# Performance work log

Hardware: AMD Instinct MI355X
Metric: run time of the kernel (lower is better)

Reference implementation:

```python
import jax, jax.numpy as jnp
import numpy as np

L, T, F, DIM = 16, 16384, 2, 3
N_MIN, N_MAX = 16.0, 512.0
N_PTS = 262144
# torch code builds np.int32 primes [1, 2654435761, 805459861]; 2654435761 wraps to -1640531535.
# Since T is a power of two, int32 wraparound multiply/xor followed by nonnegative mod T gives
# bit-identical indices to the int64 torch computation.
PIS = jnp.array([1, -1640531535, 805459861], dtype=jnp.int32)
# corner ordering from get_indices: corner k = a*4+b*2+c with a->dim0, b->dim1, c->dim2
OFFS = jnp.array([[(k >> 2) & 1, (k >> 1) & 1, k & 1] for k in range(8)], dtype=jnp.float32)  # (8,3)


def setup_inputs() -> dict:
    key = jax.random.key(0)
    k1, k2 = jax.random.split(key)
    x = jax.random.uniform(k1, (N_PTS, DIM), dtype=jnp.float32)
    # nn.init.uniform_(weight, a=-1e-4, b=1e-4) for each of L tables of shape (T, F)
    embeddings = jax.random.uniform(k2, (L, T, F), minval=-1e-4, maxval=1e-4, dtype=jnp.float32)
    return {"x": x, "embeddings": embeddings}


def reference(x, embeddings):
    # per-level growth factor b = exp((log Nmax - log Nmin)/L); N_l = Nmin * b**l
    b = jnp.exp((jnp.log(N_MAX) - jnp.log(N_MIN)) / L)
    N_l = N_MIN * b ** jnp.arange(L, dtype=jnp.float32)                      # (L,)
    un_x = x[None, :, :] * N_l[:, None, None]                                # (L,N,3)  (mu=0, sigma=1)
    lo = jnp.floor(un_x)
    hi = jnp.ceil(un_x)
    d = hi - lo                                                              # (L,N,3)
    nz = d != 0
    diff = jnp.where(nz, (un_x - lo) / jnp.where(nz, d, 1.0), 0.0)           # (L,N,3)

    mask = OFFS.astype(bool)[None, None]                                     # (1,1,8,3)
    corners = jnp.where(mask, hi[:, :, None, :], lo[:, :, None, :])          # (L,N,8,3)
    ci = corners.astype(jnp.int32)
    prod = ci * PIS                                                          # (L,N,8,3) wrapping int32 mul
    idx = jnp.mod(prod[..., 0] ^ prod[..., 1] ^ prod[..., 2], T)             # (L,N,8)

    # per-level table gather: (L,T,F)[ (L,N,8) ] -> (L,N,8,F)
    feats = jax.vmap(lambda emb, i: emb[i])(embeddings, idx)

    # trilinear weights: prod over dims of (diff if corner bit else 1-diff)
    w = jnp.prod(jnp.where(mask, diff[:, :, None, :], 1.0 - diff[:, :, None, :]), axis=-1)  # (L,N,8)
    c = jnp.einsum('lnc,lncf->lnf', w, feats)                                # (L,N,F)
    return jnp.transpose(c, (1, 0, 2)).reshape(x.shape[0], L * F)            # (N, L*F)
```

## Files before the change

kernel.cpp:

```cpp
#include <hip/hip_runtime.h>
#include <stdint.h>

constexpr int L_LEVELS = 16;
constexpr int T_SIZE   = 16384;
constexpr int N_PTS    = 262144;

typedef _Float16 h2 __attribute__((ext_vector_type(2)));
typedef _Float16 h4 __attribute__((ext_vector_type(4)));
typedef _Float16 h8 __attribute__((ext_vector_type(8)));

constexpr uint32_t P1_4 = 2654435761u * 4u;
constexpr uint32_t P2_4 = 805459861u * 4u;
constexpr uint32_t M4   = (T_SIZE - 1) * 4u;

__device__ __forceinline__ h2 lerp2(h2 a, h2 b, h2 t) {
    return a + t * (b - a);
}


__global__ __launch_bounds__(256) void cvt_tables(
    const float* __restrict__ emb, h2* __restrict__ tbl)
{
    const int i = blockIdx.x * 256 + threadIdx.x;
    const float4* __restrict__ s = reinterpret_cast<const float4*>(emb);
    float4 a = s[2 * i];
    float4 b = s[2 * i + 1];
    h8 w = { (_Float16)a.x, (_Float16)a.y, (_Float16)a.z, (_Float16)a.w,
             (_Float16)b.x, (_Float16)b.y, (_Float16)b.z, (_Float16)b.w };
    reinterpret_cast<h8*>(tbl)[i] = w;
}

__global__ __launch_bounds__(512, 4) void hash_encode_level(
    const float* __restrict__ x,
    const h2*    __restrict__ tbl,
    h2*          __restrict__ res)
{
    __shared__ h2 tab[T_SIZE];

    const int t     = threadIdx.x;
    const int l     = blockIdx.x & (L_LEVELS - 1);
    const int chunk = blockIdx.x >> 4;
    const int n0    = chunk * 4096 + t * 8;

    {
        const h8* __restrict__ s =
            reinterpret_cast<const h8*>(tbl + (size_t)l * T_SIZE);
        h8* __restrict__ d = reinterpret_cast<h8*>(tab);
#pragma unroll
        for (int r = 0; r < 8; ++r) {
            const int j = r * 512 + t;
            d[j] = s[j];
        }
    }

    union { float4 q[6]; float f[24]; } xs;
    {
        const float4* __restrict__ xv =
            reinterpret_cast<const float4*>(x + (size_t)n0 * 3);
#pragma unroll
        for (int i = 0; i < 6; ++i) xs.q[i] = xv[i];
    }
    __syncthreads();

    const float Nl = 16.0f * exp2f((float)l * 0.3125f);
    const char* __restrict__ tb = reinterpret_cast<const char*>(tab);

    union { h2 r[8]; float4 q[2]; } out8;

#pragma unroll
    for (int p = 0; p < 8; ++p) {
        const float u0 = xs.f[3 * p + 0] * Nl;
        const float u1 = xs.f[3 * p + 1] * Nl;
        const float u2 = xs.f[3 * p + 2] * Nl;

        const float fl0 = floorf(u0), fl1 = floorf(u1), fl2 = floorf(u2);
        const float df0 = u0 - fl0, df1 = u1 - fl1, df2 = u2 - fl2;

        const uint32_t q0 = ((uint32_t)(int32_t)fl0) << 2;
        const uint32_t q1 = ((uint32_t)(int32_t)fl1) * P1_4;
        const uint32_t q2 = ((uint32_t)(int32_t)fl2) * P2_4;
        const uint32_t d0 = (q0 ^ (q0 + 4u))   & M4;
        const uint32_t d1 = (q1 ^ (q1 + P1_4)) & M4;
        const uint32_t d2 = (q2 ^ (q2 + P2_4)) & M4;

        uint32_t off = (q0 ^ q1 ^ q2) & M4;

        constexpr int gray[8] = {0, 1, 3, 2, 6, 7, 5, 4};
        h2 f[8];
#pragma unroll
        for (int j = 0; j < 8; ++j) {
            f[gray[j]] = *reinterpret_cast<const h2*>(tb + off);
            if (j < 7) {
                const int tog = gray[j] ^ gray[j + 1];
                off ^= (tog == 4) ? d0 : (tog == 2) ? d1 : d2;
            }
        }

        const _Float16 h0 = (_Float16)df0, h1 = (_Float16)df1,
                       hv2 = (_Float16)df2;
        const h2 t0 = {h0, h0}, t1 = {h1, h1}, t2 = {hv2, hv2};
        h2 e0 = lerp2(f[0], f[1], t2);
        h2 e1 = lerp2(f[2], f[3], t2);
        h2 e2 = lerp2(f[4], f[5], t2);
        h2 e3 = lerp2(f[6], f[7], t2);
        h2 g0 = lerp2(e0, e1, t1);
        h2 g1 = lerp2(e2, e3, t1);
        out8.r[p] = lerp2(g0, g1, t0);
    }

    {
        float4* __restrict__ o4 = reinterpret_cast<float4*>(
            res + (size_t)l * N_PTS + n0);
        o4[0] = out8.q[0];
        o4[1] = out8.q[1];
    }
}

__global__ __launch_bounds__(256) void transpose_expand(
    const h2* __restrict__ res,
    float4*   __restrict__ out)
{
    __shared__ h2 tile[L_LEVELS][514];
    const int t    = threadIdx.x;
    const int base = blockIdx.x * 512;

#pragma unroll
    for (int l = 0; l < L_LEVELS; ++l) {
        h4 v = reinterpret_cast<const h4*>(res + (size_t)l * N_PTS + base)[t];
        *reinterpret_cast<h4*>(&tile[l][2 * t]) = v;
    }
    __syncthreads();

    float4* __restrict__ o = out + (size_t)base * 8;
#pragma unroll
    for (int i = 0; i < L_LEVELS; ++i) {
        const int f    = i * 256 + t;
        const int p    = f >> 3;
        const int part = f & 7;
        h2 a = tile[2 * part][p];
        h2 b = tile[2 * part + 1][p];
        o[f] = make_float4((float)a.x, (float)a.y,
                           (float)b.x, (float)b.y);
    }
}

__global__ __launch_bounds__(1024, 4) void hash_encode_fused(
    const float* __restrict__ x,
    const float* __restrict__ emb,
    float4*      __restrict__ out)
{
    __shared__ union {
        h2 tab[2][T_SIZE];
        h2 tr[1024][20];
    } sm;

    const int t = threadIdx.x;
    const int n = blockIdx.x * 1024 + t;
    const int rot = (blockIdx.x << 4) & 4095;

    const float x0 = x[3 * n + 0];
    const float x1 = x[3 * n + 1];
    const float x2 = x[3 * n + 2];

    {
        const float4* __restrict__ s = reinterpret_cast<const float4*>(emb);
        h8* __restrict__ d = reinterpret_cast<h8*>(sm.tab[0]);
#pragma unroll
        for (int r = 0; r < 4; ++r) {
            const int j = (r * 1024 + t + rot) & 4095;
            float4 a = s[2 * j];
            float4 b = s[2 * j + 1];
            h8 w = { (_Float16)a.x, (_Float16)a.y, (_Float16)a.z, (_Float16)a.w,
                     (_Float16)b.x, (_Float16)b.y, (_Float16)b.z, (_Float16)b.w };
            d[j] = w;
        }
    }
    __syncthreads();

    union { h2 r[L_LEVELS]; h8 q[4]; } resu;

#pragma unroll
    for (int l = 0; l < L_LEVELS; ++l) {
        float4 sa0, sb0, sa1, sb1, sa2, sb2, sa3, sb3;
        int j0 = 0, j1 = 0, j2 = 0, j3 = 0;
        if (l < L_LEVELS - 1) {
            const float4* __restrict__ s = reinterpret_cast<const float4*>(
                emb + (size_t)(l + 1) * T_SIZE * 2);
            j0 = (0 * 1024 + t + rot) & 4095;
            j1 = (1 * 1024 + t + rot) & 4095;
            j2 = (2 * 1024 + t + rot) & 4095;
            j3 = (3 * 1024 + t + rot) & 4095;
            sa0 = s[2 * j0]; sb0 = s[2 * j0 + 1];
            sa1 = s[2 * j1]; sb1 = s[2 * j1 + 1];
            sa2 = s[2 * j2]; sb2 = s[2 * j2 + 1];
            sa3 = s[2 * j3]; sb3 = s[2 * j3 + 1];
        }

        const float Nl = 16.0f * exp2f((float)l * 0.3125f);
        const char* __restrict__ tb =
            reinterpret_cast<const char*>(sm.tab[l & 1]);

        const float u0 = x0 * Nl, u1 = x1 * Nl, u2 = x2 * Nl;
        const float fl0 = floorf(u0), fl1 = floorf(u1), fl2 = floorf(u2);
        const float df0 = u0 - fl0, df1 = u1 - fl1, df2 = u2 - fl2;

        const uint32_t q0 = ((uint32_t)(int32_t)fl0) << 2;
        const uint32_t q1 = ((uint32_t)(int32_t)fl1) * P1_4;
        const uint32_t q2 = ((uint32_t)(int32_t)fl2) * P2_4;
        const uint32_t d0 = (q0 ^ (q0 + 4u))   & M4;
        const uint32_t d1 = (q1 ^ (q1 + P1_4)) & M4;
        const uint32_t d2 = (q2 ^ (q2 + P2_4)) & M4;

        uint32_t off = (q0 ^ q1 ^ q2) & M4;

        constexpr int gray[8] = {0, 1, 3, 2, 6, 7, 5, 4};
        h2 f[8];
#pragma unroll
        for (int j = 0; j < 8; ++j) {
            f[gray[j]] = *reinterpret_cast<const h2*>(tb + off);
            if (j < 7) {
                const int tog = gray[j] ^ gray[j + 1];
                off ^= (tog == 4) ? d0 : (tog == 2) ? d1 : d2;
            }
        }

        const _Float16 h0 = (_Float16)df0, h1 = (_Float16)df1, hv2 = (_Float16)df2;
        const h2 t0 = {h0, h0}, t1 = {h1, h1}, t2 = {hv2, hv2};
        h2 e0 = lerp2(f[0], f[1], t2);
        h2 e1 = lerp2(f[2], f[3], t2);
        h2 e2 = lerp2(f[4], f[5], t2);
        h2 e3 = lerp2(f[6], f[7], t2);
        h2 g0 = lerp2(e0, e1, t1);
        h2 g1 = lerp2(e2, e3, t1);
        resu.r[l] = lerp2(g0, g1, t0);

        if (l < L_LEVELS - 1) {
            h8* __restrict__ d = reinterpret_cast<h8*>(sm.tab[(l + 1) & 1]);
            h8 w0 = { (_Float16)sa0.x, (_Float16)sa0.y, (_Float16)sa0.z, (_Float16)sa0.w,
                      (_Float16)sb0.x, (_Float16)sb0.y, (_Float16)sb0.z, (_Float16)sb0.w };
            h8 w1 = { (_Float16)sa1.x, (_Float16)sa1.y, (_Float16)sa1.z, (_Float16)sa1.w,
                      (_Float16)sb1.x, (_Float16)sb1.y, (_Float16)sb1.z, (_Float16)sb1.w };
            h8 w2 = { (_Float16)sa2.x, (_Float16)sa2.y, (_Float16)sa2.z, (_Float16)sa2.w,
                      (_Float16)sb2.x, (_Float16)sb2.y, (_Float16)sb2.z, (_Float16)sb2.w };
            h8 w3 = { (_Float16)sa3.x, (_Float16)sa3.y, (_Float16)sa3.z, (_Float16)sa3.w,
                      (_Float16)sb3.x, (_Float16)sb3.y, (_Float16)sb3.z, (_Float16)sb3.w };
            d[j0] = w0;
            d[j1] = w1;
            d[j2] = w2;
            d[j3] = w3;
            __syncthreads();
        }
    }

    __syncthreads();
#pragma unroll
    for (int g = 0; g < 4; ++g)
        *reinterpret_cast<h8*>(&sm.tr[t][4 * g]) = resu.q[g];
    __syncthreads();

    float4* __restrict__ o = out + (size_t)blockIdx.x * 8192;
#pragma unroll
    for (int i = 0; i < 8; ++i) {
        const int p  = i * 128 + (t >> 3);
        const int l0 = 2 * (t & 7);
        h4 v = *reinterpret_cast<const h4*>(&sm.tr[p][l0]);
        o[i * 1024 + t] = make_float4((float)v.x, (float)v.y,
                                      (float)v.z, (float)v.w);
    }
}

extern "C" void kernel_launch(void* const* d_in, const int* in_sizes, int n_in,
                              void* d_out, int out_size, void* d_ws, size_t ws_size,
                              hipStream_t stream) {
    const float* x   = (const float*)d_in[0];
    const float* emb = (const float*)d_in[1];

    const size_t RES_OFF = (size_t)2 << 20;
    const size_t need    = RES_OFF + (size_t)L_LEVELS * N_PTS * sizeof(h2);

    if (ws_size >= need) {
        h2* tbl = (h2*)d_ws;
        h2* res = (h2*)((char*)d_ws + RES_OFF);
        cvt_tables<<<256, 256, 0, stream>>>(emb, tbl);
        hash_encode_level<<<1024, 512, 0, stream>>>(x, tbl, res);
        transpose_expand<<<512, 256, 0, stream>>>(res, (float4*)d_out);
    } else {
        hash_encode_fused<<<256, 1024, 0, stream>>>(x, emb, (float4*)d_out);
    }
}
```

Baseline: 87.38 us.

## Fuse fp16 table conversion into LDS fill and pair point lookups

```diff
diff --git a/kernel.cpp b/kernel.cpp
--- a/kernel.cpp
+++ b/kernel.cpp
@@ -18,38 +18,30 @@
 }
 
 
-__global__ __launch_bounds__(256) void cvt_tables(
-    const float* __restrict__ emb, h2* __restrict__ tbl)
-{
-    const int i = blockIdx.x * 256 + threadIdx.x;
-    const float4* __restrict__ s = reinterpret_cast<const float4*>(emb);
-    float4 a = s[2 * i];
-    float4 b = s[2 * i + 1];
-    h8 w = { (_Float16)a.x, (_Float16)a.y, (_Float16)a.z, (_Float16)a.w,
-             (_Float16)b.x, (_Float16)b.y, (_Float16)b.z, (_Float16)b.w };
-    reinterpret_cast<h8*>(tbl)[i] = w;
-}
-
-__global__ __launch_bounds__(512, 4) void hash_encode_level(
+__global__ __launch_bounds__(512, 4) void hash_encode_lds(
     const float* __restrict__ x,
-    const h2*    __restrict__ tbl,
+    const float* __restrict__ emb,
     h2*          __restrict__ res)
 {
     __shared__ h2 tab[T_SIZE];
 
-    const int t     = threadIdx.x;
     const int l     = blockIdx.x & (L_LEVELS - 1);
     const int chunk = blockIdx.x >> 4;
+    const int t     = threadIdx.x;
     const int n0    = chunk * 4096 + t * 8;
 
     {
-        const h8* __restrict__ s =
-            reinterpret_cast<const h8*>(tbl + (size_t)l * T_SIZE);
-        h8* __restrict__ d = reinterpret_cast<h8*>(tab);
-#pragma unroll
-        for (int r = 0; r < 8; ++r) {
-            const int j = r * 512 + t;
-            d[j] = s[j];
+        const float4* __restrict__ src =
+            reinterpret_cast<const float4*>(emb + (size_t)l * T_SIZE * 2);
+        h8* __restrict__ d8 = reinterpret_cast<h8*>(tab);
+#pragma unroll
+        for (int it = 0; it < 8; ++it) {
+            const int i = it * 512 + t;
+            float4 a = src[2 * i];
+            float4 b = src[2 * i + 1];
+            h8 w = { (_Float16)a.x, (_Float16)a.y, (_Float16)a.z, (_Float16)a.w,
+                     (_Float16)b.x, (_Float16)b.y, (_Float16)b.z, (_Float16)b.w };
+            d8[i] = w;
         }
     }
 
@@ -68,44 +60,59 @@
     union { h2 r[8]; float4 q[2]; } out8;
 
 #pragma unroll
-    for (int p = 0; p < 8; ++p) {
-        const float u0 = xs.f[3 * p + 0] * Nl;
-        const float u1 = xs.f[3 * p + 1] * Nl;
-        const float u2 = xs.f[3 * p + 2] * Nl;
-
-        const float fl0 = floorf(u0), fl1 = floorf(u1), fl2 = floorf(u2);
-        const float df0 = u0 - fl0, df1 = u1 - fl1, df2 = u2 - fl2;
-
-        const uint32_t q0 = ((uint32_t)(int32_t)fl0) << 2;
-        const uint32_t q1 = ((uint32_t)(int32_t)fl1) * P1_4;
-        const uint32_t q2 = ((uint32_t)(int32_t)fl2) * P2_4;
-        const uint32_t d0 = (q0 ^ (q0 + 4u))   & M4;
-        const uint32_t d1 = (q1 ^ (q1 + P1_4)) & M4;
-        const uint32_t d2 = (q2 ^ (q2 + P2_4)) & M4;
-
-        uint32_t off = (q0 ^ q1 ^ q2) & M4;
-
-        constexpr int gray[8] = {0, 1, 3, 2, 6, 7, 5, 4};
-        h2 f[8];
-#pragma unroll
-        for (int j = 0; j < 8; ++j) {
-            f[gray[j]] = *reinterpret_cast<const h2*>(tb + off);
-            if (j < 7) {
-                const int tog = gray[j] ^ gray[j + 1];
-                off ^= (tog == 4) ? d0 : (tog == 2) ? d1 : d2;
+    for (int pp = 0; pp < 8; pp += 2) {
+        uint32_t off[2], dd0[2], dd1[2], dd2[2];
+        h2 tt0[2], tt1[2], tt2[2];
+#pragma unroll
+        for (int k = 0; k < 2; ++k) {
+            const int p = pp + k;
+            const float u0 = xs.f[3 * p + 0] * Nl;
+            const float u1 = xs.f[3 * p + 1] * Nl;
+            const float u2 = xs.f[3 * p + 2] * Nl;
+
+            const float fl0 = floorf(u0), fl1 = floorf(u1), fl2 = floorf(u2);
+            const float df0 = u0 - fl0, df1 = u1 - fl1, df2 = u2 - fl2;
+
+            const uint32_t q0 = ((uint32_t)(int32_t)fl0) << 2;
+            const uint32_t q1 = ((uint32_t)(int32_t)fl1) * P1_4;
+            const uint32_t q2 = ((uint32_t)(int32_t)fl2) * P2_4;
+            dd0[k] = (q0 ^ (q0 + 4u))   & M4;
+            dd1[k] = (q1 ^ (q1 + P1_4)) & M4;
+            dd2[k] = (q2 ^ (q2 + P2_4)) & M4;
+            off[k] = (q0 ^ q1 ^ q2) & M4;
+
+            const _Float16 h0 = (_Float16)df0, h1 = (_Float16)df1,
+                           hv2 = (_Float16)df2;
+            tt0[k] = h2{h0, h0};
+            tt1[k] = h2{h1, h1};
+            tt2[k] = h2{hv2, hv2};
+        }
+
+        h2 f[2][8];
+#pragma unroll
+        for (int k = 0; k < 2; ++k) {
+            constexpr int gray[8] = {0, 1, 3, 2, 6, 7, 5, 4};
+            uint32_t o = off[k];
+#pragma unroll
+            for (int j = 0; j < 8; ++j) {
+                f[k][gray[j]] = *reinterpret_cast<const h2*>(tb + o);
+                if (j < 7) {
+                    const int tog = gray[j] ^ gray[j + 1];
+                    o ^= (tog == 4) ? dd0[k] : (tog == 2) ? dd1[k] : dd2[k];
+                }
             }
         }
 
-        const _Float16 h0 = (_Float16)df0, h1 = (_Float16)df1,
-                       hv2 = (_Float16)df2;
-        const h2 t0 = {h0, h0}, t1 = {h1, h1}, t2 = {hv2, hv2};
-        h2 e0 = lerp2(f[0], f[1], t2);
-        h2 e1 = lerp2(f[2], f[3], t2);
-        h2 e2 = lerp2(f[4], f[5], t2);
-        h2 e3 = lerp2(f[6], f[7], t2);
-        h2 g0 = lerp2(e0, e1, t1);
-        h2 g1 = lerp2(e2, e3, t1);
-        out8.r[p] = lerp2(g0, g1, t0);
+#pragma unroll
+        for (int k = 0; k < 2; ++k) {
+            h2 e0 = lerp2(f[k][0], f[k][1], tt2[k]);
+            h2 e1 = lerp2(f[k][2], f[k][3], tt2[k]);
+            h2 e2 = lerp2(f[k][4], f[k][5], tt2[k]);
+            h2 e3 = lerp2(f[k][6], f[k][7], tt2[k]);
+            h2 g0 = lerp2(e0, e1, tt1[k]);
+            h2 g1 = lerp2(e2, e3, tt1[k]);
+            out8.r[pp + k] = lerp2(g0, g1, tt0[k]);
+        }
     }
 
     {
@@ -275,14 +282,11 @@
     const float* x   = (const float*)d_in[0];
     const float* emb = (const float*)d_in[1];
 
-    const size_t RES_OFF = (size_t)2 << 20;
-    const size_t need    = RES_OFF + (size_t)L_LEVELS * N_PTS * sizeof(h2);
+    const size_t need = (size_t)L_LEVELS * N_PTS * sizeof(h2);
 
     if (ws_size >= need) {
-        h2* tbl = (h2*)d_ws;
-        h2* res = (h2*)((char*)d_ws + RES_OFF);
-        cvt_tables<<<256, 256, 0, stream>>>(emb, tbl);
-        hash_encode_level<<<1024, 512, 0, stream>>>(x, tbl, res);
+        h2* res = (h2*)d_ws;
+        hash_encode_lds<<<1024, 512, 0, stream>>>(x, emb, res);
         transpose_expand<<<512, 256, 0, stream>>>(res, (float4*)d_out);
     } else {
         hash_encode_fused<<<256, 1024, 0, stream>>>(x, emb, (float4*)d_out);
```

New measurement: 87.29 us. No clear change (-0.1%).

## Fuse level encode and transpose into one kernel with async LDS table staging

Applied to the files above, without the earlier changes.

```diff
diff --git a/kernel.cpp b/kernel.cpp
--- a/kernel.cpp
+++ b/kernel.cpp
@@ -30,49 +30,52 @@
     reinterpret_cast<h8*>(tbl)[i] = w;
 }
 
-__global__ __launch_bounds__(512, 4) void hash_encode_level(
+__global__ __launch_bounds__(1024, 4) void hash_encode_dma(
     const float* __restrict__ x,
     const h2*    __restrict__ tbl,
-    h2*          __restrict__ res)
+    float4*      __restrict__ out)
 {
-    __shared__ h2 tab[T_SIZE];
-
-    const int t     = threadIdx.x;
-    const int l     = blockIdx.x & (L_LEVELS - 1);
-    const int chunk = blockIdx.x >> 4;
-    const int n0    = chunk * 4096 + t * 8;
-
-    {
-        const h8* __restrict__ s =
-            reinterpret_cast<const h8*>(tbl + (size_t)l * T_SIZE);
-        h8* __restrict__ d = reinterpret_cast<h8*>(tab);
-#pragma unroll
-        for (int r = 0; r < 8; ++r) {
-            const int j = r * 512 + t;
-            d[j] = s[j];
-        }
-    }
-
-    union { float4 q[6]; float f[24]; } xs;
-    {
-        const float4* __restrict__ xv =
-            reinterpret_cast<const float4*>(x + (size_t)n0 * 3);
-#pragma unroll
-        for (int i = 0; i < 6; ++i) xs.q[i] = xv[i];
-    }
-    __syncthreads();
-
-    const float Nl = 16.0f * exp2f((float)l * 0.3125f);
-    const char* __restrict__ tb = reinterpret_cast<const char*>(tab);
-
-    union { h2 r[8]; float4 q[2]; } out8;
-
-#pragma unroll
-    for (int p = 0; p < 8; ++p) {
-        const float u0 = xs.f[3 * p + 0] * Nl;
-        const float u1 = xs.f[3 * p + 1] * Nl;
-        const float u2 = xs.f[3 * p + 2] * Nl;
-
+    __shared__ union {
+        h2 tab[2][T_SIZE];
+        h2 tr[1024][18];
+    } sm;
+
+    const int t    = threadIdx.x;
+    const int lane = t & 63;
+    const int wid  = t >> 6;
+    const int n    = blockIdx.x * 1024 + t;
+
+    const float x0 = x[3 * n + 0];
+    const float x1 = x[3 * n + 1];
+    const float x2 = x[3 * n + 2];
+
+    const char* __restrict__ gt = reinterpret_cast<const char*>(tbl);
+
+    auto stage = [&](int lvl, int b) {
+        const char* g = gt + ((size_t)lvl << 16) + (wid << 12) + (lane << 4);
+        char* d = reinterpret_cast<char*>(sm.tab[b]) + (wid << 12);
+#pragma unroll
+        for (int it = 0; it < 4; ++it)
+            __builtin_amdgcn_global_load_lds(
+                (const __attribute__((address_space(1))) void*)(g + (it << 10)),
+                (__attribute__((address_space(3))) void*)(d + (it << 10)),
+                16, 0, 0);
+    };
+
+    stage(0, 0);
+    __syncthreads();
+
+    union { h2 r[L_LEVELS]; h4 q4[8]; } res;
+
+#pragma unroll
+    for (int l = 0; l < L_LEVELS; ++l) {
+        if (l < L_LEVELS - 1) stage(l + 1, (l + 1) & 1);
+
+        const float Nl = 16.0f * exp2f((float)l * 0.3125f);
+        const char* __restrict__ tb =
+            reinterpret_cast<const char*>(sm.tab[l & 1]);
+
+        const float u0 = x0 * Nl, u1 = x1 * Nl, u2 = x2 * Nl;
         const float fl0 = floorf(u0), fl1 = floorf(u1), fl2 = floorf(u2);
         const float df0 = u0 - fl0, df1 = u1 - fl1, df2 = u2 - fl2;
 
@@ -105,42 +108,25 @@
         h2 e3 = lerp2(f[6], f[7], t2);
         h2 g0 = lerp2(e0, e1, t1);
         h2 g1 = lerp2(e2, e3, t1);
-        out8.r[p] = lerp2(g0, g1, t0);
-    }
-
-    {
-        float4* __restrict__ o4 = reinterpret_cast<float4*>(
-            res + (size_t)l * N_PTS + n0);
-        o4[0] = out8.q[0];
-        o4[1] = out8.q[1];
-    }
-}
-
-__global__ __launch_bounds__(256) void transpose_expand(
-    const h2* __restrict__ res,
-    float4*   __restrict__ out)
-{
-    __shared__ h2 tile[L_LEVELS][514];
-    const int t    = threadIdx.x;
-    const int base = blockIdx.x * 512;
-
-#pragma unroll
-    for (int l = 0; l < L_LEVELS; ++l) {
-        h4 v = reinterpret_cast<const h4*>(res + (size_t)l * N_PTS + base)[t];
-        *reinterpret_cast<h4*>(&tile[l][2 * t]) = v;
-    }
-    __syncthreads();
-
-    float4* __restrict__ o = out + (size_t)base * 8;
-#pragma unroll
-    for (int i = 0; i < L_LEVELS; ++i) {
-        const int f    = i * 256 + t;
+        res.r[l] = lerp2(g0, g1, t0);
+
+        __syncthreads();
+    }
+
+#pragma unroll
+    for (int g = 0; g < 8; ++g)
+        *reinterpret_cast<h4*>(&sm.tr[t][2 * g]) = res.q4[g];
+    __syncthreads();
+
+    float4* __restrict__ o = out + (size_t)blockIdx.x * 8192;
+#pragma unroll
+    for (int i = 0; i < 8; ++i) {
+        const int f    = i * 1024 + t;
         const int p    = f >> 3;
         const int part = f & 7;
-        h2 a = tile[2 * part][p];
-        h2 b = tile[2 * part + 1][p];
-        o[f] = make_float4((float)a.x, (float)a.y,
-                           (float)b.x, (float)b.y);
+        h4 v = *reinterpret_cast<const h4*>(&sm.tr[p][2 * part]);
+        o[f] = make_float4((float)v.x, (float)v.y,
+                           (float)v.z, (float)v.w);
     }
 }
 
@@ -275,15 +261,12 @@
     const float* x   = (const float*)d_in[0];
     const float* emb = (const float*)d_in[1];
 
-    const size_t RES_OFF = (size_t)2 << 20;
-    const size_t need    = RES_OFF + (size_t)L_LEVELS * N_PTS * sizeof(h2);
-
-    if (ws_size >= need) {
+    const size_t tbl_bytes = (size_t)L_LEVELS * T_SIZE * sizeof(h2);
+
+    if (ws_size >= tbl_bytes) {
         h2* tbl = (h2*)d_ws;
-        h2* res = (h2*)((char*)d_ws + RES_OFF);
         cvt_tables<<<256, 256, 0, stream>>>(emb, tbl);
-        hash_encode_level<<<1024, 512, 0, stream>>>(x, tbl, res);
-        transpose_expand<<<512, 256, 0, stream>>>(res, (float4*)d_out);
+        hash_encode_dma<<<256, 1024, 0, stream>>>(x, tbl, (float4*)d_out);
     } else {
         hash_encode_fused<<<256, 1024, 0, stream>>>(x, emb, (float4*)d_out);
     }
```

Result: slower. 98.79 us (+13.0%).
